# Optimization experiments

Measured on AMD Instinct MI355X. Metric: run time of the kernel, lower is better.

## Reference

```python
import jax, jax.numpy as jnp
import numpy as np

B, N, D, H = 4, 512, 256, 256


def setup_inputs() -> dict:
    key = jax.random.key(0)
    ks = jax.random.split(key, 8)
    s = lambda fan: 1.0 / np.sqrt(fan)
    return {
        "X": jax.random.normal(ks[0], (B, N, D), dtype=jnp.float32),
        "Y": jax.random.normal(ks[1], (B, N, D), dtype=jnp.float32),
        # fc = Linear(D,H) -> Tanh -> Linear(H,H)
        "W1": jax.random.normal(ks[2], (H, D), dtype=jnp.float32) * s(D),
        "b1": jnp.zeros((H,), dtype=jnp.float32),
        "W2": jax.random.normal(ks[3], (H, H), dtype=jnp.float32) * s(H),
        "b2": jnp.zeros((H,), dtype=jnp.float32),
        # fc_q, fc_k
        "Wq": jax.random.normal(ks[4], (H, H), dtype=jnp.float32) * s(H),
        "bq": jnp.zeros((H,), dtype=jnp.float32),
        "Wk": jax.random.normal(ks[5], (H, H), dtype=jnp.float32) * s(H),
        "bk": jnp.zeros((H,), dtype=jnp.float32),
        # AddComp projection vector v: E_ij = v . tanh(Q_i + K_j)
        "v": jax.random.normal(ks[6], (H,), dtype=jnp.float32) * s(H),
        "k": 5,
    }


def reference(X, Y, W1, b1, W2, b2, Wq, bq, Wk, bk, v, k):
    # fc: Linear -> Tanh -> Linear  (Y and k are unused, as in the original)
    h = jnp.tanh(jnp.einsum('bnd,hd->bnh', X, W1) + b1)
    h = jnp.einsum('bnh,gh->bng', h, W2) + b2          # [B,N,H]
    Q = jnp.einsum('bnh,gh->bng', h, Wq) + bq          # [B,N,H]
    K = jnp.einsum('bnh,gh->bng', h, Wk) + bk          # [B,N,H]
    # Additive compatibility: E[b,i,j] = v . tanh(Q[b,i] + K[b,j])
    E = jnp.einsum('bijh,h->bij', jnp.tanh(Q[:, :, None, :] + K[:, None, :, :]), v)
    # Symmetrize
    return 0.5 * (E + jnp.swapaxes(E, -2, -1))
```

## Files before the change

kernel.cpp:

```cpp
#include <hip/hip_runtime.h>


typedef float f2 __attribute__((ext_vector_type(2)));
typedef float f4 __attribute__((ext_vector_type(4)));
typedef float f32x4 __attribute__((ext_vector_type(4)));
typedef __bf16 bf16x8 __attribute__((ext_vector_type(8)));

#define C2F 2.8853900817779268f
#define S8  0.00390625f

__device__ inline unsigned short f2bf(float f) {
    unsigned u = __float_as_uint(f);
    unsigned r = (u + 0x7fffu + ((u >> 16) & 1u)) >> 16;
    return (unsigned short)r;
}
__device__ inline float bf2f(unsigned short h) {
    return __uint_as_float(((unsigned)h) << 16);
}

__device__ inline void split4(const f4 a, unsigned short* hp, unsigned short* lp) {
    unsigned short h[4], l[4];
#pragma unroll
    for (int t = 0; t < 4; ++t) {
        h[t] = f2bf(a[t]);
        l[t] = f2bf(a[t] - bf2f(h[t]));
    }
    uint2 hv, lv;
    hv.x = (unsigned)h[0] | ((unsigned)h[1] << 16);
    hv.y = (unsigned)h[2] | ((unsigned)h[3] << 16);
    lv.x = (unsigned)l[0] | ((unsigned)l[1] << 16);
    lv.y = (unsigned)l[2] | ((unsigned)l[3] << 16);
    *(uint2*)hp = hv;
    *(uint2*)lp = lv;
}

template <int ACT>
__global__ __launch_bounds__(256) void gemm_fullk(
    const float* __restrict__ A, const float* __restrict__ Wa,
    const float* __restrict__ Wb, const float* __restrict__ ba,
    const float* __restrict__ bb2, float* __restrict__ C, int Nn) {
    __shared__ unsigned short sAhi[64][264];
    __shared__ unsigned short sAlo[64][264];
    __shared__ unsigned short sBhi[64][264];
    __shared__ unsigned short sBlo[64][264];

    const int tid = threadIdx.x;
    const int m0 = blockIdx.x << 6;
    const int n0 = blockIdx.y << 6;

    const float* Atile = A + (size_t)m0 * 256;
    const float* Wtile = (n0 < 256) ? (Wa + (size_t)n0 * 256)
                                    : (Wb + (size_t)(n0 - 256) * 256);
    const int col4 = (tid & 63) << 2;
    const int rgrp = tid >> 6;
#pragma unroll
    for (int t = 0; t < 16; ++t) {
        const int row = (t << 2) + rgrp;
        f4 av = *(const f4*)&Atile[(size_t)row * 256 + col4];
        f4 wv = *(const f4*)&Wtile[(size_t)row * 256 + col4];
        split4(av, &sAhi[row][col4], &sAlo[row][col4]);
        split4(wv, &sBhi[row][col4], &sBlo[row][col4]);
    }
    __syncthreads();

    const int lane = tid & 63;
    const int wav = tid >> 6;
    const int wm = wav >> 1, wn = wav & 1;
    const int fr = lane & 15;
    const int fks = (lane >> 4) << 3;

    f32x4 acc[2][2];
#pragma unroll
    for (int i = 0; i < 2; ++i)
#pragma unroll
        for (int j = 0; j < 2; ++j) acc[i][j] = (f32x4){0.f, 0.f, 0.f, 0.f};

#pragma unroll
    for (int kt = 0; kt < 256; kt += 32) {
        bf16x8 ah[2], al[2], bh[2], bl[2];
#pragma unroll
        for (int s = 0; s < 2; ++s) {
            ah[s] = *(const bf16x8*)&sAhi[(wm << 5) + (s << 4) + fr][kt + fks];
            al[s] = *(const bf16x8*)&sAlo[(wm << 5) + (s << 4) + fr][kt + fks];
            bh[s] = *(const bf16x8*)&sBhi[(wn << 5) + (s << 4) + fr][kt + fks];
            bl[s] = *(const bf16x8*)&sBlo[(wn << 5) + (s << 4) + fr][kt + fks];
        }
#pragma unroll
        for (int i = 0; i < 2; ++i)
#pragma unroll
            for (int j = 0; j < 2; ++j) {
                acc[i][j] = __builtin_amdgcn_mfma_f32_16x16x32_bf16(ah[i], bh[j], acc[i][j], 0, 0, 0);
                acc[i][j] = __builtin_amdgcn_mfma_f32_16x16x32_bf16(ah[i], bl[j], acc[i][j], 0, 0, 0);
                acc[i][j] = __builtin_amdgcn_mfma_f32_16x16x32_bf16(al[i], bh[j], acc[i][j], 0, 0, 0);
            }
    }

    const int rbase = (lane >> 4) << 2;
#pragma unroll
    for (int i = 0; i < 2; ++i) {
#pragma unroll
        for (int j = 0; j < 2; ++j) {
            const int gcol = n0 + (wn << 5) + (j << 4) + fr;
            const float bias = (ACT == 2 && gcol >= 256) ? bb2[gcol - 256] : ba[gcol];
#pragma unroll
            for (int q = 0; q < 4; ++q) {
                const int grow = m0 + (wm << 5) + (i << 4) + rbase + q;
                float x = acc[i][j][q] + bias;
                if (ACT == 1)
                    x = 1.0f - 2.0f * __builtin_amdgcn_rcpf(
                                          1.0f + __builtin_amdgcn_exp2f(C2F * x));
                if (ACT == 2) {
                    if (gcol < 256)
                        x = fminf(__builtin_amdgcn_exp2f(C2F * x - 8.0f), 4.0f);
                    else
                        x = fminf(__builtin_amdgcn_exp2f(C2F * x), 1024.0f);
                }
                C[(size_t)grow * Nn + gcol] = x;
            }
        }
    }
}

__global__ __launch_bounds__(256) void gemm_stage1(
    const float* __restrict__ X, const float* __restrict__ W1,
    const float* __restrict__ b1, const float* __restrict__ Wq,
    const float* __restrict__ Wk, const float* __restrict__ W2,
    const float* __restrict__ b2, const float* __restrict__ bq,
    const float* __restrict__ bk, float* __restrict__ h1,
    float* __restrict__ Wc, float* __restrict__ bc,
    float* __restrict__ Ep) {
    __shared__ unsigned short sAhi[64][264];
    __shared__ unsigned short sAlo[64][264];
    __shared__ unsigned short sBhi[64][264];
    __shared__ unsigned short sBlo[64][264];
    __shared__ float sred[64][4];

    const int tid = threadIdx.x;

    if (blockIdx.x >= 160) {
        const int zb = blockIdx.x - 160;
        f4* dst = (f4*)(Ep + (size_t)zb * 16384) + tid;
        const f4 z = (f4){0.f, 0.f, 0.f, 0.f};
#pragma unroll
        for (int t = 0; t < 16; ++t) dst[t * 256] = z;
        return;
    }

    const bool is_nt = (blockIdx.x >= 128);
    const int blk = is_nt ? (blockIdx.x - 128) : blockIdx.x;
    const int m0 = (blk >> 2) << 6;
    const int n0 = (blk & 3) << 6;

    const int col4 = (tid & 63) << 2;
    const int rgrp = tid >> 6;

    if (!is_nt) {
        const float* Atile = X + (size_t)m0 * 256;
        const float* Wtile = W1 + (size_t)n0 * 256;
#pragma unroll
        for (int t = 0; t < 16; ++t) {
            const int row = (t << 2) + rgrp;
            f4 av = *(const f4*)&Atile[(size_t)row * 256 + col4];
            f4 wv = *(const f4*)&Wtile[(size_t)row * 256 + col4];
            split4(av, &sAhi[row][col4], &sAlo[row][col4]);
            split4(wv, &sBhi[row][col4], &sBlo[row][col4]);
        }
    } else {
        const float* Atile = (m0 < 256) ? (Wq + (size_t)m0 * 256)
                                        : (Wk + (size_t)(m0 - 256) * 256);
#pragma unroll
        for (int t = 0; t < 16; ++t) {
            const int row = (t << 2) + rgrp;
            f4 av = *(const f4*)&Atile[(size_t)row * 256 + col4];
            split4(av, &sAhi[row][col4], &sAlo[row][col4]);
        }
        const int c4 = (tid & 15) << 2;
        const int kg = tid >> 4;
#pragma unroll
        for (int t = 0; t < 16; ++t) {
            const int k = (t << 4) + kg;
            f4 wv = *(const f4*)&W2[(size_t)k * 256 + n0 + c4];
#pragma unroll
            for (int q = 0; q < 4; ++q) {
                unsigned short hi = f2bf(wv[q]);
                sBhi[c4 + q][k] = hi;
                sBlo[c4 + q][k] = f2bf(wv[q] - bf2f(hi));
            }
        }
    }
    __syncthreads();

    const int lane = tid & 63;
    const int wav = tid >> 6;
    const int wm = wav >> 1, wn = wav & 1;
    const int fr = lane & 15;
    const int fks = (lane >> 4) << 3;

    f32x4 acc[2][2];
#pragma unroll
    for (int i = 0; i < 2; ++i)
#pragma unroll
        for (int j = 0; j < 2; ++j) acc[i][j] = (f32x4){0.f, 0.f, 0.f, 0.f};

#pragma unroll
    for (int kt = 0; kt < 256; kt += 32) {
        bf16x8 ah[2], al[2], bh[2], bl[2];
#pragma unroll
        for (int s = 0; s < 2; ++s) {
            ah[s] = *(const bf16x8*)&sAhi[(wm << 5) + (s << 4) + fr][kt + fks];
            al[s] = *(const bf16x8*)&sAlo[(wm << 5) + (s << 4) + fr][kt + fks];
            bh[s] = *(const bf16x8*)&sBhi[(wn << 5) + (s << 4) + fr][kt + fks];
            bl[s] = *(const bf16x8*)&sBlo[(wn << 5) + (s << 4) + fr][kt + fks];
        }
#pragma unroll
        for (int i = 0; i < 2; ++i)
#pragma unroll
            for (int j = 0; j < 2; ++j) {
                acc[i][j] = __builtin_amdgcn_mfma_f32_16x16x32_bf16(ah[i], bh[j], acc[i][j], 0, 0, 0);
                acc[i][j] = __builtin_amdgcn_mfma_f32_16x16x32_bf16(ah[i], bl[j], acc[i][j], 0, 0, 0);
                acc[i][j] = __builtin_amdgcn_mfma_f32_16x16x32_bf16(al[i], bh[j], acc[i][j], 0, 0, 0);
            }
    }

    const int rbase = (lane >> 4) << 2;
    if (!is_nt) {
#pragma unroll
        for (int i = 0; i < 2; ++i)
#pragma unroll
            for (int j = 0; j < 2; ++j) {
                const int gcol = n0 + (wn << 5) + (j << 4) + fr;
                const float bias = b1[gcol];
#pragma unroll
                for (int q = 0; q < 4; ++q) {
                    const int grow = m0 + (wm << 5) + (i << 4) + rbase + q;
                    float x = acc[i][j][q] + bias;
                    x = 1.0f - 2.0f * __builtin_amdgcn_rcpf(
                                          1.0f + __builtin_amdgcn_exp2f(C2F * x));
                    h1[(size_t)grow * 256 + gcol] = x;
                }
            }
    } else {
#pragma unroll
        for (int i = 0; i < 2; ++i)
#pragma unroll
            for (int j = 0; j < 2; ++j) {
                const int gcol = n0 + (wn << 5) + (j << 4) + fr;
#pragma unroll
                for (int q = 0; q < 4; ++q) {
                    const int grow = m0 + (wm << 5) + (i << 4) + rbase + q;
                    Wc[(size_t)grow * 256 + gcol] = acc[i][j][q];
                }
            }
        if ((blk & 3) == 0) {
            const int rr = tid >> 2;
            const int part = (tid & 3) << 6;
            const int grow = m0 + rr;
            const float* Ar = (grow < 256) ? &Wq[(size_t)grow * 256]
                                           : &Wk[(size_t)(grow - 256) * 256];
            float s = 0.f;
#pragma unroll
            for (int e = 0; e < 64; e += 4) {
                f4 a = *(const f4*)&Ar[part + e];
                f4 bv = *(const f4*)&b2[part + e];
                s += a[0] * bv[0] + a[1] * bv[1] + a[2] * bv[2] + a[3] * bv[3];
            }
            sred[rr][tid & 3] = s;
            __syncthreads();
            if (tid < 64) {
                float bias = sred[tid][0] + sred[tid][1] + sred[tid][2] + sred[tid][3];
                const int g2 = m0 + tid;
                bias += (g2 < 256) ? bq[g2] : bk[g2 - 256];
                bc[g2] = bias;
            }
        }
    }
}

__global__ __launch_bounds__(512, 4) void pairwise_kernel(
    const float* __restrict__ uwb, const float* __restrict__ v,
    float* __restrict__ Ep) {
    __shared__ float sU[64][68];
    __shared__ float sW[64][68];
    __shared__ float sV[64];

    const int tid = threadIdx.x;
    const int bb = blockIdx.x;
    const int hcs = bb & 3;
    const int hc = hcs << 6;
    const int tt = bb >> 2;
    const int b = tt >> 6;
    const int i0 = ((tt >> 3) & 7) << 6;
    const int j0 = (tt & 7) << 6;

    const float* ubase = uwb + (size_t)((b << 9) + i0) * 512 + hc;
    const float* wbase = uwb + (size_t)((b << 9) + j0) * 512 + 256 + hc;

    const int sr = tid >> 3;
    const int sc = (tid & 7) << 3;
    {
        f4 a0 = *(const f4*)&ubase[(size_t)sr * 512 + sc];
        f4 a1 = *(const f4*)&ubase[(size_t)sr * 512 + sc + 4];
        f4 b0 = *(const f4*)&wbase[(size_t)sr * 512 + sc];
        f4 b1 = *(const f4*)&wbase[(size_t)sr * 512 + sc + 4];
        *(f4*)&sU[sr][sc] = a0;
        *(f4*)&sU[sr][sc + 4] = a1;
        *(f4*)&sW[sr][sc] = b0;
        *(f4*)&sW[sr][sc + 4] = b1;
    }
    if (tid < 16) *(f4*)&sV[tid << 2] = *(const f4*)&v[hc + (tid << 2)];
    __syncthreads();

    const int ty = tid >> 5;
    const int tx = tid & 31;

    float acc[4][2];
#pragma unroll
    for (int d = 0; d < 4; ++d)
#pragma unroll
        for (int e = 0; e < 2; ++e) acc[d][e] = 0.f;

#pragma unroll 2
    for (int h8 = 0; h8 < 64; h8 += 8) {
        const f4 vv0 = *(const f4*)&sV[h8];
        const f4 vv1 = *(const f4*)&sV[h8 + 4];
        f4 w0[2], w1[2];
#pragma unroll
        for (int e = 0; e < 2; ++e) {
            w0[e] = *(const f4*)&sW[tx + (e << 5)][h8];
            w1[e] = *(const f4*)&sW[tx + (e << 5)][h8 + 4];
        }
#pragma unroll
        for (int d = 0; d < 4; ++d) {
            const f4 u0 = *(const f4*)&sU[ty + (d << 4)][h8];
            const f4 u1 = *(const f4*)&sU[ty + (d << 4)][h8 + 4];
#pragma unroll
            for (int e = 0; e < 2; ++e) {
                const float A0 = fmaf(u0.x, w0[e].x, S8);
                const float A1 = fmaf(u0.y, w0[e].y, S8);
                const float A2 = fmaf(u0.z, w0[e].z, S8);
                const float A3 = fmaf(u0.w, w0[e].w, S8);
                const float A4 = fmaf(u1.x, w1[e].x, S8);
                const float A5 = fmaf(u1.y, w1[e].y, S8);
                const float A6 = fmaf(u1.z, w1[e].z, S8);
                const float A7 = fmaf(u1.w, w1[e].w, S8);
                const float m01 = A0 * A1, m23 = A2 * A3;
                const float m45 = A4 * A5, m67 = A6 * A7;
                const float t01 = fmaf(vv0.x, A1, vv0.y * A0);
                const float t23 = fmaf(vv0.z, A3, vv0.w * A2);
                const float t45 = fmaf(vv1.x, A5, vv1.y * A4);
                const float t67 = fmaf(vv1.z, A7, vv1.w * A6);
                const float m03 = m01 * m23, m47 = m45 * m67;
                const float t03 = fmaf(t01, m23, t23 * m01);
                const float t47 = fmaf(t45, m67, t67 * m45);
                const float M = m03 * m47;
                const float N = fmaf(t03, m47, t47 * m03);
                acc[d][e] = fmaf(N, __builtin_amdgcn_rcpf(M), acc[d][e]);
            }
        }
    }

    float* ep = Ep + (size_t)((b << 9) + i0) * 512 + j0;
#pragma unroll
    for (int d = 0; d < 4; ++d)
#pragma unroll
        for (int e = 0; e < 2; ++e)
            atomicAdd(&ep[(size_t)(ty + (d << 4)) * 512 + tx + (e << 5)],
                      acc[d][e] * S8);
}

__global__ __launch_bounds__(256) void sym_kernel(const float* __restrict__ Ep,
                                                  const float* __restrict__ v,
                                                  float* __restrict__ out) {
    __shared__ float t1[64][65];
    __shared__ float t2[64][65];
    __shared__ float red[4];

    const int tid = threadIdx.x;
    const int lane = tid & 63, wv = tid >> 6;

    float x = v[tid];
#pragma unroll
    for (int o = 32; o > 0; o >>= 1) x += __shfl_xor(x, o, 64);
    if (lane == 0) red[wv] = x;

    const int bb = blockIdx.x;
    const int b = bb >> 6;
    const int i0 = ((bb >> 3) & 7) << 6;
    const int j0 = (bb & 7) << 6;

    for (int idx = tid; idx < 4096; idx += 256) {
        const int r = idx >> 6, c = idx & 63;
        t1[r][c] = Ep[(size_t)((b << 9) + i0 + r) * 512 + j0 + c];
        t2[r][c] = Ep[(size_t)((b << 9) + j0 + r) * 512 + i0 + c];
    }
    __syncthreads();
    const float Sv = red[0] + red[1] + red[2] + red[3];
    for (int idx = tid; idx < 4096; idx += 256) {
        const int r = idx >> 6, c = idx & 63;
        out[(size_t)((b << 9) + i0 + r) * 512 + j0 + c] = Sv - (t1[r][c] + t2[c][r]);
    }
}

extern "C" void kernel_launch(void* const* d_in, const int* in_sizes, int n_in,
                              void* d_out, int out_size, void* d_ws, size_t ws_size,
                              hipStream_t stream) {
    const float* X  = (const float*)d_in[0];
    const float* W1 = (const float*)d_in[2];
    const float* b1 = (const float*)d_in[3];
    const float* W2 = (const float*)d_in[4];
    const float* b2 = (const float*)d_in[5];
    const float* Wq = (const float*)d_in[6];
    const float* bq = (const float*)d_in[7];
    const float* Wk = (const float*)d_in[8];
    const float* bk = (const float*)d_in[9];
    const float* v  = (const float*)d_in[10];

    float* ws  = (float*)d_ws;
    float* h1  = ws;
    float* uwb = ws + 524288;
    float* Wc  = ws + 1572864;
    float* bc  = ws + 1703936;
    float* Ep  = ws + 1704448;
    float* out = (float*)d_out;

    gemm_stage1<<<224, 256, 0, stream>>>(X, W1, b1, Wq, Wk, W2, b2, bq, bk,
                                         h1, Wc, bc, Ep);
    gemm_fullk<2><<<dim3(32, 8), 256, 0, stream>>>(h1, Wc, Wc + 65536, bc,
                                                   bc + 256, uwb, 512);
    pairwise_kernel<<<1024, 512, 0, stream>>>(uwb, v, Ep);
    sym_kernel<<<256, 256, 0, stream>>>(Ep, v, out);
}
```

Measured before the change: 57.44 us.

## Shrink GEMM tiles to 64x32 and stage K in two halves

Both GEMM kernels now use 64x32 output tiles and load K in two 128-wide halves instead of staging the full 256-wide K at once. This cuts shared memory per block roughly fourfold and doubles the grid (stage1 goes from 224 to 384 blocks, gemm2 from 256 to 512), so more blocks can be resident and more CUs get work. The cost is an extra barrier pair per block and more redundant loading and bf16 splitting of the A tiles across the N blocks. The pairwise kernel's inner math is moved into a macro with no change in behaviour.

```diff
diff --git a/kernel.cpp b/kernel.cpp
--- a/kernel.cpp
+++ b/kernel.cpp
@@ -1,7 +1,6 @@
 #include <hip/hip_runtime.h>
 
 
-typedef float f2 __attribute__((ext_vector_type(2)));
 typedef float f4 __attribute__((ext_vector_type(4)));
 typedef float f32x4 __attribute__((ext_vector_type(4)));
 typedef __bf16 bf16x8 __attribute__((ext_vector_type(8)));
@@ -34,34 +33,23 @@
     *(uint2*)lp = lv;
 }
 
-template <int ACT>
-__global__ __launch_bounds__(256) void gemm_fullk(
+
+__global__ __launch_bounds__(256) void gemm2_kernel(
     const float* __restrict__ A, const float* __restrict__ Wa,
     const float* __restrict__ Wb, const float* __restrict__ ba,
-    const float* __restrict__ bb2, float* __restrict__ C, int Nn) {
-    __shared__ unsigned short sAhi[64][264];
-    __shared__ unsigned short sAlo[64][264];
-    __shared__ unsigned short sBhi[64][264];
-    __shared__ unsigned short sBlo[64][264];
+    const float* __restrict__ bb2, float* __restrict__ C) {
+    __shared__ unsigned short sAhi[64][136];
+    __shared__ unsigned short sAlo[64][136];
+    __shared__ unsigned short sBhi[32][136];
+    __shared__ unsigned short sBlo[32][136];
 
     const int tid = threadIdx.x;
     const int m0 = blockIdx.x << 6;
-    const int n0 = blockIdx.y << 6;
-
-    const float* Atile = A + (size_t)m0 * 256;
-    const float* Wtile = (n0 < 256) ? (Wa + (size_t)n0 * 256)
-                                    : (Wb + (size_t)(n0 - 256) * 256);
-    const int col4 = (tid & 63) << 2;
-    const int rgrp = tid >> 6;
-#pragma unroll
-    for (int t = 0; t < 16; ++t) {
-        const int row = (t << 2) + rgrp;
-        f4 av = *(const f4*)&Atile[(size_t)row * 256 + col4];
-        f4 wv = *(const f4*)&Wtile[(size_t)row * 256 + col4];
-        split4(av, &sAhi[row][col4], &sAlo[row][col4]);
-        split4(wv, &sBhi[row][col4], &sBlo[row][col4]);
-    }
-    __syncthreads();
+    const int n0 = blockIdx.y << 5;
+
+    const float* Arow = A + (size_t)m0 * 256;
+    const float* Wrow = (n0 < 256) ? (Wa + (size_t)n0 * 256)
+                                   : (Wb + (size_t)(n0 - 256) * 256);
 
     const int lane = tid & 63;
     const int wav = tid >> 6;
@@ -69,54 +57,64 @@
     const int fr = lane & 15;
     const int fks = (lane >> 4) << 3;
 
-    f32x4 acc[2][2];
-#pragma unroll
-    for (int i = 0; i < 2; ++i)
-#pragma unroll
-        for (int j = 0; j < 2; ++j) acc[i][j] = (f32x4){0.f, 0.f, 0.f, 0.f};
-
-#pragma unroll
-    for (int kt = 0; kt < 256; kt += 32) {
-        bf16x8 ah[2], al[2], bh[2], bl[2];
-#pragma unroll
-        for (int s = 0; s < 2; ++s) {
-            ah[s] = *(const bf16x8*)&sAhi[(wm << 5) + (s << 4) + fr][kt + fks];
-            al[s] = *(const bf16x8*)&sAlo[(wm << 5) + (s << 4) + fr][kt + fks];
-            bh[s] = *(const bf16x8*)&sBhi[(wn << 5) + (s << 4) + fr][kt + fks];
-            bl[s] = *(const bf16x8*)&sBlo[(wn << 5) + (s << 4) + fr][kt + fks];
-        }
-#pragma unroll
-        for (int i = 0; i < 2; ++i)
-#pragma unroll
-            for (int j = 0; j < 2; ++j) {
-                acc[i][j] = __builtin_amdgcn_mfma_f32_16x16x32_bf16(ah[i], bh[j], acc[i][j], 0, 0, 0);
-                acc[i][j] = __builtin_amdgcn_mfma_f32_16x16x32_bf16(ah[i], bl[j], acc[i][j], 0, 0, 0);
-                acc[i][j] = __builtin_amdgcn_mfma_f32_16x16x32_bf16(al[i], bh[j], acc[i][j], 0, 0, 0);
-            }
+    f32x4 acc[2];
+    acc[0] = (f32x4){0.f, 0.f, 0.f, 0.f};
+    acc[1] = (f32x4){0.f, 0.f, 0.f, 0.f};
+
+    const int sa_r = tid >> 2, sa_c = (tid & 3) << 5;
+    const int sb_r = tid >> 3, sb_c = (tid & 7) << 4;
+
+#pragma unroll
+    for (int kh = 0; kh < 2; ++kh) {
+        const int kb = kh << 7;
+#pragma unroll
+        for (int t = 0; t < 8; ++t) {
+            const int c = sa_c + (t << 2);
+            f4 av = *(const f4*)&Arow[(size_t)sa_r * 256 + kb + c];
+            split4(av, &sAhi[sa_r][c], &sAlo[sa_r][c]);
+        }
+#pragma unroll
+        for (int t = 0; t < 4; ++t) {
+            const int c = sb_c + (t << 2);
+            f4 wv = *(const f4*)&Wrow[(size_t)sb_r * 256 + kb + c];
+            split4(wv, &sBhi[sb_r][c], &sBlo[sb_r][c]);
+        }
+        __syncthreads();
+
+#pragma unroll
+        for (int kt = 0; kt < 128; kt += 32) {
+            bf16x8 ah[2], al[2], bh, bl;
+#pragma unroll
+            for (int s = 0; s < 2; ++s) {
+                ah[s] = *(const bf16x8*)&sAhi[(wm << 5) + (s << 4) + fr][kt + fks];
+                al[s] = *(const bf16x8*)&sAlo[(wm << 5) + (s << 4) + fr][kt + fks];
+            }
+            bh = *(const bf16x8*)&sBhi[(wn << 4) + fr][kt + fks];
+            bl = *(const bf16x8*)&sBlo[(wn << 4) + fr][kt + fks];
+#pragma unroll
+            for (int s = 0; s < 2; ++s) {
+                acc[s] = __builtin_amdgcn_mfma_f32_16x16x32_bf16(ah[s], bh, acc[s], 0, 0, 0);
+                acc[s] = __builtin_amdgcn_mfma_f32_16x16x32_bf16(ah[s], bl, acc[s], 0, 0, 0);
+                acc[s] = __builtin_amdgcn_mfma_f32_16x16x32_bf16(al[s], bh, acc[s], 0, 0, 0);
+            }
+        }
+        __syncthreads();
     }
 
     const int rbase = (lane >> 4) << 2;
-#pragma unroll
-    for (int i = 0; i < 2; ++i) {
-#pragma unroll
-        for (int j = 0; j < 2; ++j) {
-            const int gcol = n0 + (wn << 5) + (j << 4) + fr;
-            const float bias = (ACT == 2 && gcol >= 256) ? bb2[gcol - 256] : ba[gcol];
-#pragma unroll
-            for (int q = 0; q < 4; ++q) {
-                const int grow = m0 + (wm << 5) + (i << 4) + rbase + q;
-                float x = acc[i][j][q] + bias;
-                if (ACT == 1)
-                    x = 1.0f - 2.0f * __builtin_amdgcn_rcpf(
-                                          1.0f + __builtin_amdgcn_exp2f(C2F * x));
-                if (ACT == 2) {
-                    if (gcol < 256)
-                        x = fminf(__builtin_amdgcn_exp2f(C2F * x - 8.0f), 4.0f);
-                    else
-                        x = fminf(__builtin_amdgcn_exp2f(C2F * x), 1024.0f);
-                }
-                C[(size_t)grow * Nn + gcol] = x;
-            }
+    const int gcol = n0 + (wn << 4) + fr;
+    const float bias = (gcol >= 256) ? bb2[gcol - 256] : ba[gcol];
+#pragma unroll
+    for (int s = 0; s < 2; ++s) {
+#pragma unroll
+        for (int q = 0; q < 4; ++q) {
+            const int grow = m0 + (wm << 5) + (s << 4) + rbase + q;
+            float x = acc[s][q] + bias;
+            if (gcol < 256)
+                x = fminf(__builtin_amdgcn_exp2f(C2F * x - 8.0f), 4.0f);
+            else
+                x = fminf(__builtin_amdgcn_exp2f(C2F * x), 1024.0f);
+            C[(size_t)grow * 512 + gcol] = x;
         }
     }
 }
@@ -127,18 +125,17 @@
     const float* __restrict__ Wk, const float* __restrict__ W2,
     const float* __restrict__ b2, const float* __restrict__ bq,
     const float* __restrict__ bk, float* __restrict__ h1,
-    float* __restrict__ Wc, float* __restrict__ bc,
-    float* __restrict__ Ep) {
-    __shared__ unsigned short sAhi[64][264];
-    __shared__ unsigned short sAlo[64][264];
-    __shared__ unsigned short sBhi[64][264];
-    __shared__ unsigned short sBlo[64][264];
+    float* __restrict__ Wc, float* __restrict__ bc, float* __restrict__ Ep) {
+    __shared__ unsigned short sAhi[64][136];
+    __shared__ unsigned short sAlo[64][136];
+    __shared__ unsigned short sBhi[32][136];
+    __shared__ unsigned short sBlo[32][136];
     __shared__ float sred[64][4];
 
     const int tid = threadIdx.x;
 
-    if (blockIdx.x >= 160) {
-        const int zb = blockIdx.x - 160;
+    if (blockIdx.x >= 320) {
+        const int zb = blockIdx.x - 320;
         f4* dst = (f4*)(Ep + (size_t)zb * 16384) + tid;
         const f4 z = (f4){0.f, 0.f, 0.f, 0.f};
 #pragma unroll
@@ -146,49 +143,19 @@
         return;
     }
 
-    const bool is_nt = (blockIdx.x >= 128);
-    const int blk = is_nt ? (blockIdx.x - 128) : blockIdx.x;
-    const int m0 = (blk >> 2) << 6;
-    const int n0 = (blk & 3) << 6;
-
-    const int col4 = (tid & 63) << 2;
-    const int rgrp = tid >> 6;
-
+    const bool is_nt = (blockIdx.x >= 256);
+    const int blk = is_nt ? (blockIdx.x - 256) : blockIdx.x;
+    const int m0 = (blk >> 3) << 6;
+    const int n0 = (blk & 7) << 5;
+
+    const float* Arow;
     if (!is_nt) {
-        const float* Atile = X + (size_t)m0 * 256;
-        const float* Wtile = W1 + (size_t)n0 * 256;
-#pragma unroll
-        for (int t = 0; t < 16; ++t) {
-            const int row = (t << 2) + rgrp;
-            f4 av = *(const f4*)&Atile[(size_t)row * 256 + col4];
-            f4 wv = *(const f4*)&Wtile[(size_t)row * 256 + col4];
-            split4(av, &sAhi[row][col4], &sAlo[row][col4]);
-            split4(wv, &sBhi[row][col4], &sBlo[row][col4]);
-        }
+        Arow = X + (size_t)m0 * 256;
     } else {
-        const float* Atile = (m0 < 256) ? (Wq + (size_t)m0 * 256)
-                                        : (Wk + (size_t)(m0 - 256) * 256);
-#pragma unroll
-        for (int t = 0; t < 16; ++t) {
-            const int row = (t << 2) + rgrp;
-            f4 av = *(const f4*)&Atile[(size_t)row * 256 + col4];
-            split4(av, &sAhi[row][col4], &sAlo[row][col4]);
-        }
-        const int c4 = (tid & 15) << 2;
-        const int kg = tid >> 4;
-#pragma unroll
-        for (int t = 0; t < 16; ++t) {
-            const int k = (t << 4) + kg;
-            f4 wv = *(const f4*)&W2[(size_t)k * 256 + n0 + c4];
-#pragma unroll
-            for (int q = 0; q < 4; ++q) {
-                unsigned short hi = f2bf(wv[q]);
-                sBhi[c4 + q][k] = hi;
-                sBlo[c4 + q][k] = f2bf(wv[q] - bf2f(hi));
-            }
-        }
-    }
-    __syncthreads();
+        Arow = (m0 < 256) ? (Wq + (size_t)m0 * 256)
+                          : (Wk + (size_t)(m0 - 256) * 256);
+    }
+    const float* W1row = W1 + (size_t)n0 * 256;
 
     const int lane = tid & 63;
     const int wav = tid >> 6;
@@ -196,62 +163,91 @@
     const int fr = lane & 15;
     const int fks = (lane >> 4) << 3;
 
-    f32x4 acc[2][2];
-#pragma unroll
-    for (int i = 0; i < 2; ++i)
-#pragma unroll
-        for (int j = 0; j < 2; ++j) acc[i][j] = (f32x4){0.f, 0.f, 0.f, 0.f};
-
-#pragma unroll
-    for (int kt = 0; kt < 256; kt += 32) {
-        bf16x8 ah[2], al[2], bh[2], bl[2];
+    f32x4 acc[2];
+    acc[0] = (f32x4){0.f, 0.f, 0.f, 0.f};
+    acc[1] = (f32x4){0.f, 0.f, 0.f, 0.f};
+
+    const int sa_r = tid >> 2, sa_c = (tid & 3) << 5;
+    const int sb_r = tid >> 3, sb_c = (tid & 7) << 4;
+    const int nt_c = (tid & 7) << 2;
+    const int nt_k = tid >> 3;
+
+#pragma unroll
+    for (int kh = 0; kh < 2; ++kh) {
+        const int kb = kh << 7;
+#pragma unroll
+        for (int t = 0; t < 8; ++t) {
+            const int c = sa_c + (t << 2);
+            f4 av = *(const f4*)&Arow[(size_t)sa_r * 256 + kb + c];
+            split4(av, &sAhi[sa_r][c], &sAlo[sa_r][c]);
+        }
+        if (!is_nt) {
+#pragma unroll
+            for (int t = 0; t < 4; ++t) {
+                const int c = sb_c + (t << 2);
+                f4 wv = *(const f4*)&W1row[(size_t)sb_r * 256 + kb + c];
+                split4(wv, &sBhi[sb_r][c], &sBlo[sb_r][c]);
+            }
+        } else {
+#pragma unroll
+            for (int t = 0; t < 4; ++t) {
+                const int k = (t << 5) + nt_k;
+                f4 wv = *(const f4*)&W2[(size_t)(kb + k) * 256 + n0 + nt_c];
+#pragma unroll
+                for (int q = 0; q < 4; ++q) {
+                    unsigned short hi = f2bf(wv[q]);
+                    sBhi[nt_c + q][k] = hi;
+                    sBlo[nt_c + q][k] = f2bf(wv[q] - bf2f(hi));
+                }
+            }
+        }
+        __syncthreads();
+
+#pragma unroll
+        for (int kt = 0; kt < 128; kt += 32) {
+            bf16x8 ah[2], al[2], bh, bl;
+#pragma unroll
+            for (int s = 0; s < 2; ++s) {
+                ah[s] = *(const bf16x8*)&sAhi[(wm << 5) + (s << 4) + fr][kt + fks];
+                al[s] = *(const bf16x8*)&sAlo[(wm << 5) + (s << 4) + fr][kt + fks];
+            }
+            bh = *(const bf16x8*)&sBhi[(wn << 4) + fr][kt + fks];
+            bl = *(const bf16x8*)&sBlo[(wn << 4) + fr][kt + fks];
+#pragma unroll
+            for (int s = 0; s < 2; ++s) {
+                acc[s] = __builtin_amdgcn_mfma_f32_16x16x32_bf16(ah[s], bh, acc[s], 0, 0, 0);
+                acc[s] = __builtin_amdgcn_mfma_f32_16x16x32_bf16(ah[s], bl, acc[s], 0, 0, 0);
+                acc[s] = __builtin_amdgcn_mfma_f32_16x16x32_bf16(al[s], bh, acc[s], 0, 0, 0);
+            }
+        }
+        __syncthreads();
+    }
+
+    const int rbase = (lane >> 4) << 2;
+    const int gcol = n0 + (wn << 4) + fr;
+    if (!is_nt) {
+        const float bias = b1[gcol];
 #pragma unroll
         for (int s = 0; s < 2; ++s) {
-            ah[s] = *(const bf16x8*)&sAhi[(wm << 5) + (s << 4) + fr][kt + fks];
-            al[s] = *(const bf16x8*)&sAlo[(wm << 5) + (s << 4) + fr][kt + fks];
-            bh[s] = *(const bf16x8*)&sBhi[(wn << 5) + (s << 4) + fr][kt + fks];
-            bl[s] = *(const bf16x8*)&sBlo[(wn << 5) + (s << 4) + fr][kt + fks];
-        }
-#pragma unroll
-        for (int i = 0; i < 2; ++i)
-#pragma unroll
-            for (int j = 0; j < 2; ++j) {
-                acc[i][j] = __builtin_amdgcn_mfma_f32_16x16x32_bf16(ah[i], bh[j], acc[i][j], 0, 0, 0);
-                acc[i][j] = __builtin_amdgcn_mfma_f32_16x16x32_bf16(ah[i], bl[j], acc[i][j], 0, 0, 0);
-                acc[i][j] = __builtin_amdgcn_mfma_f32_16x16x32_bf16(al[i], bh[j], acc[i][j], 0, 0, 0);
-            }
-    }
-
-    const int rbase = (lane >> 4) << 2;
-    if (!is_nt) {
-#pragma unroll
-        for (int i = 0; i < 2; ++i)
-#pragma unroll
-            for (int j = 0; j < 2; ++j) {
-                const int gcol = n0 + (wn << 5) + (j << 4) + fr;
-                const float bias = b1[gcol];
-#pragma unroll
-                for (int q = 0; q < 4; ++q) {
-                    const int grow = m0 + (wm << 5) + (i << 4) + rbase + q;
-                    float x = acc[i][j][q] + bias;
-                    x = 1.0f - 2.0f * __builtin_amdgcn_rcpf(
-                                          1.0f + __builtin_amdgcn_exp2f(C2F * x));
-                    h1[(size_t)grow * 256 + gcol] = x;
-                }
-            }
+#pragma unroll
+            for (int q = 0; q < 4; ++q) {
+                const int grow = m0 + (wm << 5) + (s << 4) + rbase + q;
+                float x = acc[s][q] + bias;
+                x = 1.0f - 2.0f * __builtin_amdgcn_rcpf(
+                                      1.0f + __builtin_amdgcn_exp2f(C2F * x));
+                h1[(size_t)grow * 256 + gcol] = x;
+            }
+        }
     } else {
 #pragma unroll
-        for (int i = 0; i < 2; ++i)
-#pragma unroll
-            for (int j = 0; j < 2; ++j) {
-                const int gcol = n0 + (wn << 5) + (j << 4) + fr;
-#pragma unroll
-                for (int q = 0; q < 4; ++q) {
-                    const int grow = m0 + (wm << 5) + (i << 4) + rbase + q;
-                    Wc[(size_t)grow * 256 + gcol] = acc[i][j][q];
-                }
-            }
-        if ((blk & 3) == 0) {
+        for (int s = 0; s < 2; ++s) {
+#pragma unroll
+            for (int q = 0; q < 4; ++q) {
+                const int grow = m0 + (wm << 5) + (s << 4) + rbase + q;
+                Wc[(size_t)grow * 256 + gcol] = acc[s][q];
+            }
+        }
+        if ((blk & 7) == 0) {
             const int rr = tid >> 2;
             const int part = (tid & 3) << 6;
             const int grow = m0 + rr;
@@ -275,6 +271,30 @@
         }
     }
 }
+
+#define TREE8(u0, u1, wv0, wv1, vv0, vv1, ACCV)                              \
+    {                                                                        \
+        const float A0 = fmaf(u0.x, wv0.x, S8);                              \
+        const float A1 = fmaf(u0.y, wv0.y, S8);                              \
+        const float A2 = fmaf(u0.z, wv0.z, S8);                              \
+        const float A3 = fmaf(u0.w, wv0.w, S8);                              \
+        const float A4 = fmaf(u1.x, wv1.x, S8);                              \
+        const float A5 = fmaf(u1.y, wv1.y, S8);                              \
+        const float A6 = fmaf(u1.z, wv1.z, S8);                              \
+        const float A7 = fmaf(u1.w, wv1.w, S8);                              \
+        const float m01 = A0 * A1, m23 = A2 * A3;                            \
+        const float m45 = A4 * A5, m67 = A6 * A7;                            \
+        const float t01 = fmaf(vv0.x, A1, vv0.y * A0);                       \
+        const float t23 = fmaf(vv0.z, A3, vv0.w * A2);                       \
+        const float t45 = fmaf(vv1.x, A5, vv1.y * A4);                       \
+        const float t67 = fmaf(vv1.z, A7, vv1.w * A6);                       \
+        const float m03 = m01 * m23, m47 = m45 * m67;                        \
+        const float t03 = fmaf(t01, m23, t23 * m01);                         \
+        const float t47 = fmaf(t45, m67, t67 * m45);                         \
+        const float M = m03 * m47;                                           \
+        const float N = fmaf(t03, m47, t47 * m03);                           \
+        ACCV = fmaf(N, __builtin_amdgcn_rcpf(M), ACCV);                      \
+    }
 
 __global__ __launch_bounds__(512, 4) void pairwise_kernel(
     const float* __restrict__ uwb, const float* __restrict__ v,
@@ -334,28 +354,7 @@
             const f4 u0 = *(const f4*)&sU[ty + (d << 4)][h8];
             const f4 u1 = *(const f4*)&sU[ty + (d << 4)][h8 + 4];
 #pragma unroll
-            for (int e = 0; e < 2; ++e) {
-                const float A0 = fmaf(u0.x, w0[e].x, S8);
-                const float A1 = fmaf(u0.y, w0[e].y, S8);
-                const float A2 = fmaf(u0.z, w0[e].z, S8);
-                const float A3 = fmaf(u0.w, w0[e].w, S8);
-                const float A4 = fmaf(u1.x, w1[e].x, S8);
-                const float A5 = fmaf(u1.y, w1[e].y, S8);
-                const float A6 = fmaf(u1.z, w1[e].z, S8);
-                const float A7 = fmaf(u1.w, w1[e].w, S8);
-                const float m01 = A0 * A1, m23 = A2 * A3;
-                const float m45 = A4 * A5, m67 = A6 * A7;
-                const float t01 = fmaf(vv0.x, A1, vv0.y * A0);
-                const float t23 = fmaf(vv0.z, A3, vv0.w * A2);
-                const float t45 = fmaf(vv1.x, A5, vv1.y * A4);
-                const float t67 = fmaf(vv1.z, A7, vv1.w * A6);
-                const float m03 = m01 * m23, m47 = m45 * m67;
-                const float t03 = fmaf(t01, m23, t23 * m01);
-                const float t47 = fmaf(t45, m67, t67 * m45);
-                const float M = m03 * m47;
-                const float N = fmaf(t03, m47, t47 * m03);
-                acc[d][e] = fmaf(N, __builtin_amdgcn_rcpf(M), acc[d][e]);
-            }
+            for (int e = 0; e < 2; ++e) TREE8(u0, u1, w0[e], w1[e], vv0, vv1, acc[d][e])
         }
     }
 
@@ -423,10 +422,10 @@
     float* Ep  = ws + 1704448;
     float* out = (float*)d_out;
 
-    gemm_stage1<<<224, 256, 0, stream>>>(X, W1, b1, Wq, Wk, W2, b2, bq, bk,
+    gemm_stage1<<<384, 256, 0, stream>>>(X, W1, b1, Wq, Wk, W2, b2, bq, bk,
                                          h1, Wc, bc, Ep);
-    gemm_fullk<2><<<dim3(32, 8), 256, 0, stream>>>(h1, Wc, Wc + 65536, bc,
-                                                   bc + 256, uwb, 512);
+    gemm2_kernel<<<dim3(32, 16), 256, 0, stream>>>(h1, Wc, Wc + 65536, bc,
+                                                   bc + 256, uwb);
     pairwise_kernel<<<1024, 512, 0, stream>>>(uwb, v, Ep);
     sym_kernel<<<256, 256, 0, stream>>>(Ep, v, out);
 }
```

Result: slower. 59.46 us (+3.5%).
